# Performance work log

Measured on AMD Instinct MI355X. Metric: run time of the kernel, lower is better.

## Reference

```python
import jax, jax.numpy as jnp
import numpy as np

N, F_IN, H, OUT, E = 50000, 128, 128, 40, 800000


def setup_inputs() -> dict:
    key = jax.random.key(0)
    ks = jax.random.split(key, 20)
    s = 0.05
    return {
        "x": jax.random.normal(ks[0], (N, F_IN), jnp.float32),
        "edge_index": jax.random.randint(ks[1], (2, E), 0, N, jnp.int64),
        # GATConv (heads=1)
        "W_gat": jax.random.normal(ks[2], (F_IN, H), jnp.float32) * s,
        "att_src": jax.random.normal(ks[3], (H,), jnp.float32) * s,
        "att_dst": jax.random.normal(ks[4], (H,), jnp.float32) * s,
        "b_gat": jnp.zeros((H,), jnp.float32),
        # GCNConv
        "W_gcn": jax.random.normal(ks[5], (F_IN, H), jnp.float32) * s,
        "b_gcn": jnp.zeros((H,), jnp.float32),
        # SAGEConv (mean aggr): lin_l on neighbors (with bias), lin_r on root (no bias)
        "W_sage_l": jax.random.normal(ks[6], (F_IN, H), jnp.float32) * s,
        "b_sage_l": jnp.zeros((H,), jnp.float32),
        "W_sage_r": jax.random.normal(ks[7], (F_IN, H), jnp.float32) * s,
        # MLP head
        "W1": jax.random.normal(ks[8], (3 * H, 2 * H), jnp.float32) * s,
        "b1": jnp.zeros((2 * H,), jnp.float32),
        "W2": jax.random.normal(ks[9], (2 * H, H), jnp.float32) * s,
        "b2": jnp.zeros((H,), jnp.float32),
        "W3": jax.random.normal(ks[10], (H, OUT), jnp.float32) * s,
        "b3": jnp.zeros((OUT,), jnp.float32),
        # BatchNorm1d(3H)
        "gamma": jnp.ones((3 * H,), jnp.float32),
        "beta": jnp.zeros((3 * H,), jnp.float32),
    }


def _add_self_loops(edge_index, n):
    loop = jnp.arange(n, dtype=edge_index.dtype)
    src = jnp.concatenate([edge_index[0], loop])
    dst = jnp.concatenate([edge_index[1], loop])
    return src, dst


def _gat(x, src, dst, n, W, att_src, att_dst, bias):
    h = x @ W                                   # [N, H]
    a_s = h @ att_src                           # [N]
    a_d = h @ att_dst                           # [N]
    e = jax.nn.leaky_relu(a_s[src] + a_d[dst], 0.2)  # [E']
    m = jax.ops.segment_max(e, dst, num_segments=n)
    ex = jnp.exp(e - m[dst])
    denom = jax.ops.segment_sum(ex, dst, num_segments=n)
    alpha = ex / denom[dst]
    out = jax.ops.segment_sum(alpha[:, None] * h[src], dst, num_segments=n)
    return out + bias


def _gcn(x, src, dst, n, W, bias):
    h = x @ W
    deg = jax.ops.segment_sum(jnp.ones_like(dst, dtype=h.dtype), dst, num_segments=n)
    dinv = jnp.where(deg > 0, jax.lax.rsqrt(deg), 0.0)
    norm = dinv[src] * dinv[dst]                # [E']
    out = jax.ops.segment_sum(norm[:, None] * h[src], dst, num_segments=n)
    return out + bias


def _sage(x, src, dst, n, W_l, b_l, W_r):
    agg = jax.ops.segment_sum(x[src], dst, num_segments=n)
    cnt = jax.ops.segment_sum(jnp.ones_like(dst, dtype=x.dtype), dst, num_segments=n)
    mean = agg / jnp.maximum(cnt, 1.0)[:, None]
    return mean @ W_l + b_l + x @ W_r


def reference(x, edge_index, W_gat, att_src, att_dst, b_gat, W_gcn, b_gcn,
              W_sage_l, b_sage_l, W_sage_r, W1, b1, W2, b2, W3, b3, gamma, beta):
    n = x.shape[0]
    src, dst = edge_index[0], edge_index[1]          # SAGE: no self-loops
    src_sl, dst_sl = _add_self_loops(edge_index, n)  # GAT/GCN add self-loops

    x_gat = _gat(x, src_sl, dst_sl, n, W_gat, att_src, att_dst, b_gat)
    x_gcn = _gcn(x, src_sl, dst_sl, n, W_gcn, b_gcn)
    x_sage = _sage(x, src, dst, n, W_sage_l, b_sage_l, W_sage_r)

    h = jnp.concatenate([x_gat, x_gcn, x_sage], axis=1)  # [N, 3H]
    # BatchNorm1d (training-mode batch statistics; biased variance, eps=1e-5)
    mu = h.mean(axis=0)
    var = h.var(axis=0)
    h = (h - mu) * jax.lax.rsqrt(var + 1e-5) * gamma + beta
    # dropout is identity at inference
    h = jax.nn.relu(h) @ W1 + b1
    h = jax.nn.relu(h) @ W2 + b2
    h = jax.nn.relu(h) @ W3 + b3
    return h
```

## Files before the change

### kernel.cpp

```cpp
#include <hip/hip_runtime.h>
#include <cstdint>
#include <cstddef>

#define NN   50000
#define FIN  128
#define HD   128
#define EE   800000
#define C3   384
#define NOUT 40

#define SC_ELEMS 512
#define SC_BLKS  ((NN + SC_ELEMS - 1) / SC_ELEMS)
#define NBLK ((NN + 127) / 128)

#define SPLIT_BLKS ((NN + 3) / 4)

#define NBUCK ((NN + 511) / 512)
#define BCAP  16384
#define BK_BLKS ((EE + 8191) / 8192)
#define SCAP  12288

#define LDSW 132

typedef __attribute__((ext_vector_type(8))) short s8v;
typedef __attribute__((ext_vector_type(4))) float f4v;
typedef __attribute__((ext_vector_type(4))) ushort u4v;

typedef const __attribute__((address_space(1))) unsigned int* guintp;
typedef __attribute__((address_space(3))) unsigned int* luintp;

static __device__ __forceinline__ void async_copy16(const void* g, void* l) {
    __builtin_amdgcn_global_load_lds((guintp)g, (luintp)l, 16, 0, 0);
}

static __device__ __forceinline__ float b2f(ushort u) {
    return __uint_as_float((unsigned)u << 16);
}
static __device__ __forceinline__ ushort f2b(float v) {
    unsigned u = __float_as_uint(v);
    unsigned r = u + 0x7fffu + ((u >> 16) & 1u);
    return (ushort)(r >> 16);
}

__global__ __launch_bounds__(256) void k_split_x_att(
    const float* __restrict__ x,
    const float* __restrict__ w_as, const float* __restrict__ w_ad,
    ushort* __restrict__ xb,
    float* __restrict__ a_s, float* __restrict__ a_d)
{
    int node = blockIdx.x * 4 + (threadIdx.x >> 6);
    if (node >= NN) return;
    int lane = threadIdx.x & 63;
    size_t o = (size_t)node * 128 + lane * 2;
    float2 v  = *(const float2*)(x + o);
    { ushort2 u; u.x = f2b(v.x); u.y = f2b(v.y); *(ushort2*)(xb + o) = u; }
    float2 w1 = *(const float2*)(w_as + lane * 2);
    float2 w2 = *(const float2*)(w_ad + lane * 2);
    float s1 = v.x * w1.x + v.y * w1.y;
    float s2 = v.x * w2.x + v.y * w2.y;
    #pragma unroll
    for (int off = 32; off; off >>= 1) {
        s1 += __shfl_down(s1, off);
        s2 += __shfl_down(s2, off);
    }
    if (lane == 0) { a_s[node] = s1; a_d[node] = s2; }
}

__global__ void k_splitw_all(
    const float* __restrict__ Wg, const float* __restrict__ Wc,
    const float* __restrict__ Wl, const float* __restrict__ Wr,
    const float* __restrict__ W1, const float* __restrict__ W2,
    const float* __restrict__ W3,
    const float* __restrict__ asv, const float* __restrict__ adv,
    float* __restrict__ w_as, float* __restrict__ w_ad,
    ushort* __restrict__ btg, ushort* __restrict__ btc,
    ushort* __restrict__ btsg,
    ushort* __restrict__ bt1, ushort* __restrict__ bt2,
    ushort* __restrict__ bt3)
{
    int ry = blockIdx.x;
    int t = threadIdx.x;
    if (ry == 816) {
        if (t < 128) {
            float s1 = 0.f, s2 = 0.f;
            for (int j = 0; j < 128; ++j) {
                float w = Wg[t * 128 + j];
                s1 += w * asv[j];
                s2 += w * adv[j];
            }
            w_as[t] = s1; w_ad[t] = s2;
        }
        return;
    }
    const float* W = nullptr; ushort* dh; int K, Nw, n;
    bool sage = false;
    if (ry < 128)      { n = ry;       K = 128; Nw = 128; W = Wg; dh = btg; }
    else if (ry < 256) { n = ry - 128; K = 128; Nw = 128; W = Wc; dh = btc; }
    else if (ry < 384) { n = ry - 256; K = 256; Nw = 128; sage = true; dh = btsg; }
    else if (ry < 640) { n = ry - 384; K = 384; Nw = 256; W = W1; dh = bt1; }
    else if (ry < 768) { n = ry - 640; K = 256; Nw = 128; W = W2; dh = bt2; }
    else               { n = ry - 768; K = 128; Nw = 40;  W = W3; dh = bt3; }
    for (int k = t; k < K; k += 256) {
        float v;
        if (sage) v = (k < 128) ? Wl[(size_t)k * 128 + n] : Wr[(size_t)(k - 128) * 128 + n];
        else      v = (n < Nw) ? W[(size_t)k * Nw + n] : 0.f;
        dh[(size_t)n * K + k] = f2b(v);
    }
}

template<int NT, int NCH, int AX>
__global__ __launch_bounds__(256, 5) void k_gemm2(
    const ushort* __restrict__ A, int K,
    const ushort* __restrict__ Bt,
    int M, int mode,
    const float* __restrict__ bias,
    float* __restrict__ Cf, int ldc,
    ushort* __restrict__ Ch, int ldch,
    int colmax)
{
    constexpr int COLS = NT * 16;
    constexpr int HOPU = 8 * COLS;
    constexpr int KTOT = NCH * 128;

    __shared__ __align__(16) ushort S[16384];
    ushort* Bs = S;
    ushort* As = S + 8192;

    const int lane = threadIdx.x & 63;
    const int wave = threadIdx.x >> 6;
    const int quad = lane >> 4;
    const int ln15 = lane & 15;
    const int brow = AX ? blockIdx.y : blockIdx.x;
    const int bcol = AX ? blockIdx.x : blockIdx.y;
    const int row0 = brow * 128 + wave * 32;
    const int col0 = bcol * COLS;
    const int Rbase = brow * 128;

    auto stageB = [&](int c, int h) {
        for (int u0 = wave * 64; u0 < HOPU; u0 += 256) {
            int u  = u0 + lane;
            int kq  = u / COLS;
            int col = u - kq * COLS;
            int kk  = c * 128 + h * 64 + kq * 8;
            const ushort* gp = Bt + (size_t)(col0 + col) * KTOT + kk;
            async_copy16(gp, (char*)Bs + (size_t)u0 * 16);
        }
    };
    auto stageA = [&](int c, int h) {
        #pragma unroll
        for (int i = 0; i < 4; ++i) {
            int u0 = (wave * 4 + i) * 64;
            int u  = u0 + lane;
            int row = u >> 3;
            int s   = u & 7;
            int sg  = s ^ (row & 7);
            int rr = Rbase + row; if (rr > M - 1) rr = M - 1;
            int kk = c * 128 + h * 64 + sg * 8;
            const ushort* gp = A + (size_t)rr * K + kk;
            async_copy16(gp, (char*)As + (size_t)u0 * 16);
        }
    };
    auto afrag = [&](int jj, int mt) -> s8v {
        int r = wave * 32 + mt * 16 + ln15;
        int sg = jj * 4 + quad;
        int unit = r * 8 + (sg ^ (r & 7));
        return *(const s8v*)(As + (size_t)unit * 8);
    };

    f4v acc[2][NT] = {};

    auto compute = [&](int jj) {
        s8v a0 = afrag(jj, 0);
        s8v a1 = afrag(jj, 1);
        #pragma unroll
        for (int t = 0; t < NT; ++t) {
            int ub = (jj * 4 + quad) * COLS + t * 16 + ln15;
            s8v b = *(const s8v*)(Bs + (size_t)ub * 8);
            acc[0][t] = __builtin_amdgcn_mfma_f32_16x16x32_bf16(a0, b, acc[0][t], 0, 0, 0);
            acc[1][t] = __builtin_amdgcn_mfma_f32_16x16x32_bf16(a1, b, acc[1][t], 0, 0, 0);
        }
    };

    stageB(0, 0); stageA(0, 0);
    __syncthreads();

    #pragma unroll
    for (int ph = 0; ph < NCH; ++ph) {
        #pragma unroll
        for (int h = 0; h < 2; ++h) {
            compute(0); compute(1);
            if (!(ph == NCH - 1 && h == 1)) {
                __syncthreads();
                int nc = ph, nh = h + 1;
                if (nh == 2) { nh = 0; ++nc; }
                stageB(nc, nh); stageA(nc, nh);
                __syncthreads();
            }
        }
    }

    if (NT == 8 && mode == 0) {
        __syncthreads();
        ushort* Lp = S + wave * 2176;
        #pragma unroll
        for (int mt = 0; mt < 2; ++mt) {
            #pragma unroll
            for (int t = 0; t < NT; ++t) {
                int cc = col0 + t * 16 + ln15;
                #pragma unroll
                for (int r = 0; r < 4; ++r) {
                    float v = acc[mt][t][r] + bias[cc];
                    v = v > 0.f ? v : 0.f;
                    Lp[(quad * 4 + r) * LDSW + t * 16 + ln15] = f2b(v);
                }
            }
            int cb = (lane & 31) * 4;
            #pragma unroll
            for (int it = 0; it < 8; ++it) {
                int row2 = it * 2 + (lane >> 5);
                int rr = row0 + mt * 16 + row2;
                uint2 v = *(uint2*)(Lp + row2 * LDSW + cb);
                if (rr < M)
                    *(uint2*)(Ch + (size_t)rr * ldch + col0 + cb) = v;
            }
        }
    } else {
        #pragma unroll
        for (int t = 0; t < NT; ++t) {
            int cc = col0 + t * 16 + ln15;
            #pragma unroll
            for (int mt = 0; mt < 2; ++mt) {
                #pragma unroll
                for (int r = 0; r < 4; ++r) {
                    int rr = row0 + mt * 16 + quad * 4 + r;
                    if (rr < M && cc < colmax)
                        Cf[(size_t)rr * ldc + cc] = acc[mt][t][r] + bias[cc];
                }
            }
        }
    }
}

__global__ __launch_bounds__(256, 3) void k_gemm_prod(
    const ushort* __restrict__ tgb, const ushort* __restrict__ tcb,
    const ushort* __restrict__ tsb, const ushort* __restrict__ xb,
    const ushort* __restrict__ btg, const ushort* __restrict__ btc,
    const ushort* __restrict__ btsg,
    const float* __restrict__ bg, const float* __restrict__ bc,
    const float* __restrict__ bsl,
    float* __restrict__ pS, float* __restrict__ pQ,
    ushort* __restrict__ hch)
{
    constexpr int COLS = 128;
    constexpr int HOPU = 8 * COLS;
    __shared__ __align__(16) ushort S[16384];
    ushort* Bs = S;
    ushort* As = S + 8192;
    float* red = (float*)(S + 14336);

    const int z = blockIdx.z;
    const ushort* A1 = (z == 0) ? tgb : (z == 1) ? tcb : tsb;
    const ushort* Bt = (z == 0) ? btg : (z == 1) ? btc : btsg;
    const float*  bias = (z == 0) ? bg : (z == 1) ? bc : bsl;
    const int nch = (z == 2) ? 2 : 1;
    const int ktot = nch * 128;

    const int lane = threadIdx.x & 63;
    const int wave = threadIdx.x >> 6;
    const int quad = lane >> 4;
    const int ln15 = lane & 15;
    const int row0 = blockIdx.x * 128 + wave * 32;
    const int Rbase = blockIdx.x * 128;

    auto stageB = [&](int c, int h) {
        for (int u0 = wave * 64; u0 < HOPU; u0 += 256) {
            int u  = u0 + lane;
            int kq  = u / COLS;
            int col = u - kq * COLS;
            int kk  = c * 128 + h * 64 + kq * 8;
            const ushort* gp = Bt + (size_t)col * ktot + kk;
            async_copy16(gp, (char*)Bs + (size_t)u0 * 16);
        }
    };
    auto stageA = [&](int c, int h) {
        #pragma unroll
        for (int i = 0; i < 4; ++i) {
            int u0 = (wave * 4 + i) * 64;
            int u  = u0 + lane;
            int row = u >> 3;
            int s   = u & 7;
            int sg  = s ^ (row & 7);
            int rr = Rbase + row; if (rr > NN - 1) rr = NN - 1;
            int kk = c * 128 + h * 64 + sg * 8;
            const ushort* gp = (kk < 128) ? (A1 + (size_t)rr * 128 + kk)
                                          : (xb + (size_t)rr * 128 + (kk - 128));
            async_copy16(gp, (char*)As + (size_t)u0 * 16);
        }
    };
    auto afrag = [&](int jj, int mt) -> s8v {
        int r = wave * 32 + mt * 16 + ln15;
        int sg = jj * 4 + quad;
        int unit = r * 8 + (sg ^ (r & 7));
        return *(const s8v*)(As + (size_t)unit * 8);
    };

    f4v acc[2][8] = {};

    auto compute = [&](int jj) {
        s8v a0 = afrag(jj, 0);
        s8v a1 = afrag(jj, 1);
        #pragma unroll
        for (int t = 0; t < 8; ++t) {
            int ub = (jj * 4 + quad) * COLS + t * 16 + ln15;
            s8v b = *(const s8v*)(Bs + (size_t)ub * 8);
            acc[0][t] = __builtin_amdgcn_mfma_f32_16x16x32_bf16(a0, b, acc[0][t], 0, 0, 0);
            acc[1][t] = __builtin_amdgcn_mfma_f32_16x16x32_bf16(a1, b, acc[1][t], 0, 0, 0);
        }
    };

    stageB(0, 0); stageA(0, 0);
    __syncthreads();

    for (int ph = 0; ph < nch; ++ph) {
        for (int h = 0; h < 2; ++h) {
            compute(0); compute(1);
            if (!(ph == nch - 1 && h == 1)) {
                __syncthreads();
                int nc = ph, nh = h + 1;
                if (nh == 2) { nh = 0; ++nc; }
                stageB(nc, nh); stageA(nc, nh);
                __syncthreads();
            }
        }
    }

    __syncthreads();
    if (threadIdx.x < 256) red[threadIdx.x] = 0.f;
    ushort* Lp = S + wave * 2176;
    float sp[8] = {}, qp[8] = {};
    #pragma unroll
    for (int mt = 0; mt < 2; ++mt) {
        #pragma unroll
        for (int t = 0; t < 8; ++t) {
            #pragma unroll
            for (int r = 0; r < 4; ++r) {
                int rr = row0 + mt * 16 + quad * 4 + r;
                float v = acc[mt][t][r] + bias[t * 16 + ln15];
                Lp[(quad * 4 + r) * LDSW + t * 16 + ln15] = f2b(v);
                if (rr < NN) { sp[t] += v; qp[t] += v * v; }
            }
        }
        int cb = (lane & 31) * 4;
        #pragma unroll
        for (int it = 0; it < 8; ++it) {
            int row2 = it * 2 + (lane >> 5);
            int rr = row0 + mt * 16 + row2;
            uint2 v = *(uint2*)(Lp + row2 * LDSW + cb);
            if (rr < NN)
                *(uint2*)(hch + (size_t)rr * C3 + z * 128 + cb) = v;
        }
    }
    __syncthreads();
    #pragma unroll
    for (int t = 0; t < 8; ++t) {
        float s = sp[t], q = qp[t];
        s += __shfl_xor(s, 16); s += __shfl_xor(s, 32);
        q += __shfl_xor(q, 16); q += __shfl_xor(q, 32);
        if (quad == 0) {
            atomicAdd(&red[t * 16 + ln15], s);
            atomicAdd(&red[128 + t * 16 + ln15], q);
        }
    }
    __syncthreads();
    if (threadIdx.x < 128) {
        size_t o = (size_t)blockIdx.x * C3 + z * 128 + threadIdx.x;
        pS[o] = red[threadIdx.x];
        pQ[o] = red[128 + threadIdx.x];
    }
}

__global__ __launch_bounds__(256) void k_scan_part(
    const int* __restrict__ degA, int* __restrict__ bsum)
{
    int t = threadIdx.x;
    int b0 = blockIdx.x * SC_ELEMS;
    int i0 = b0 + t * 2;
    int v0 = (i0 < NN)     ? degA[i0] + 1     : 0;
    int v1 = (i0 + 1 < NN) ? degA[i0 + 1] + 1 : 0;
    int s = v0 + v1;
    #pragma unroll
    for (int off = 32; off; off >>= 1) s += __shfl_down(s, off);
    __shared__ int ws[4];
    if ((t & 63) == 0) ws[t >> 6] = s;
    __syncthreads();
    if (t == 0) bsum[blockIdx.x] = ws[0] + ws[1] + ws[2] + ws[3];
}

__global__ __launch_bounds__(128) void k_scan_tops(
    const int* __restrict__ bsum, int* __restrict__ boffs)
{
    __shared__ int sh[128];
    int t = threadIdx.x;
    int v = (t < SC_BLKS) ? bsum[t] : 0;
    sh[t] = v;
    __syncthreads();
    for (int off = 1; off < 128; off <<= 1) {
        int u = (t >= off) ? sh[t - off] : 0;
        __syncthreads();
        sh[t] += u;
        __syncthreads();
    }
    if (t < SC_BLKS) boffs[t] = sh[t] - v;
    if (t == SC_BLKS - 1) boffs[SC_BLKS] = sh[t];
}

__global__ __launch_bounds__(256) void k_scan_apply(
    const int* __restrict__ degA, const int* __restrict__ boffs,
    int* __restrict__ offs, float* __restrict__ dinv)
{
    __shared__ int sh[256];
    int t = threadIdx.x;
    int b0 = blockIdx.x * SC_ELEMS;
    int i0 = b0 + t * 2;
    int v0 = (i0 < NN)     ? degA[i0] + 1     : 0;
    int v1 = (i0 + 1 < NN) ? degA[i0 + 1] + 1 : 0;
    int pair = v0 + v1;
    sh[t] = pair;
    __syncthreads();
    for (int off = 1; off < 256; off <<= 1) {
        int u = (t >= off) ? sh[t - off] : 0;
        __syncthreads();
        sh[t] += u;
        __syncthreads();
    }
    int excl = sh[t] - pair + boffs[blockIdx.x];
    if (i0 < NN) {
        offs[i0] = excl;
        dinv[i0] = rsqrtf((float)v0);
    }
    if (i0 + 1 < NN) {
        offs[i0 + 1] = excl + v0;
        dinv[i0 + 1] = rsqrtf((float)v1);
    }
    if (blockIdx.x == SC_BLKS - 1 && t == 255) offs[NN] = excl + pair;
}

__global__ __launch_bounds__(1024) void k_bucket(
    const int* __restrict__ e_src, const int* __restrict__ e_dst,
    int* __restrict__ bcnt, uint* __restrict__ ebuf)
{
    __shared__ uint sval[8192];
    __shared__ int scnt[NBUCK], sbase[NBUCK];
    int t = threadIdx.x;
    if (t < NBUCK) scnt[t] = 0;
    __syncthreads();
    int e0 = blockIdx.x * 8192;
    #pragma unroll
    for (int i = 0; i < 8; ++i) {
        int g = e0 + i * 1024 + t;
        uint val = 0xffffffffu;
        if (g < EE) {
            int d = e_dst[g];
            int s = e_src[g];
            int b = d >> 9;
            val = ((uint)b << 25) | ((uint)(d & 511) << 16) | (uint)s;
            atomicAdd(&scnt[b], 1);
        }
        sval[i * 1024 + t] = val;
    }
    __syncthreads();
    if (t < NBUCK) {
        sbase[t] = atomicAdd(&bcnt[t], scnt[t]);
        scnt[t] = 0;
    }
    __syncthreads();
    #pragma unroll
    for (int i = 0; i < 8; ++i) {
        uint val = sval[i * 1024 + t];
        if (val != 0xffffffffu) {
            int b = val >> 25;
            int lo = atomicAdd(&scnt[b], 1);
            ebuf[(size_t)b * BCAP + sbase[b] + lo] = val;
        }
    }
}

__global__ __launch_bounds__(1024) void k_deg(
    const int* __restrict__ bcnt, const uint* __restrict__ ebuf,
    int* __restrict__ degA)
{
    __shared__ int hist[512];
    int b = blockIdx.x, t = threadIdx.x;
    int d0 = b * 512;
    int ndst = NN - d0; if (ndst > 512) ndst = 512;
    if (t < 512) hist[t] = 0;
    __syncthreads();
    int nb = bcnt[b];
    const uint* eb = ebuf + (size_t)b * BCAP;
    for (int i = t; i < nb; i += 1024)
        atomicAdd(&hist[(eb[i] >> 16) & 511], 1);
    __syncthreads();
    if (t < ndst) degA[d0 + t] = hist[t];
}

__global__ __launch_bounds__(1024) void k_csr_build(
    const int* __restrict__ bcnt, const uint* __restrict__ ebuf,
    const int* __restrict__ offs, ushort* __restrict__ esrc)
{
    __shared__ ushort sout[SCAP];
    __shared__ int cur[512];
    int b = blockIdx.x, t = threadIdx.x;
    int d0 = b * 512;
    int ndst = NN - d0; if (ndst > 512) ndst = 512;
    int obase = offs[d0];
    if (t < ndst) cur[t] = offs[d0 + t] - obase;
    __syncthreads();
    int nb = bcnt[b];
    const uint* eb = ebuf + (size_t)b * BCAP;
    for (int i = t; i < nb; i += 1024) {
        uint val = eb[i];
        int slot = atomicAdd(&cur[(val >> 16) & 511], 1);
        sout[slot] = (ushort)(val & 0xffffu);
    }
    if (t < ndst) {
        int slot = atomicAdd(&cur[t], 1);
        sout[slot] = (ushort)(d0 + t);
    }
    __syncthreads();
    int total = offs[d0 + ndst] - obase;
    for (int i = t; i < total; i += 1024)
        esrc[obase + i] = sout[i];
}

__global__ __launch_bounds__(256) void k_gather(
    const ushort* __restrict__ esrc, const int* __restrict__ offs,
    const float* __restrict__ a_s, const float* __restrict__ a_d,
    const float* __restrict__ dinv,
    const ushort* __restrict__ xb,
    ushort* __restrict__ tgb, ushort* __restrict__ tcb,
    ushort* __restrict__ tsb)
{
    int d = blockIdx.x * 4 + (threadIdx.x >> 6);
    if (d >= NN) return;
    int lane = threadIdx.x & 63;
    int sub = lane & 31;
    int grp = lane >> 5;
    int beg = offs[d], end = offs[d + 1];
    float ad = a_d[d], dd = dinv[d];

    int idx0 = beg + lane;
    bool v0 = idx0 < end;
    int s0 = d; float e0 = 0.f, wc0 = 0.f;
    if (v0) {
        s0 = esrc[idx0];
        float e = a_s[s0] + ad;
        e0 = (e > 0.f) ? e : 0.2f * e;
        wc0 = dinv[s0] * dd;
    }
    float m = v0 ? e0 : -3.0e38f;
    for (int base = beg + 64; base < end; base += 64) {
        int idx = base + lane;
        if (idx < end) {
            int s = esrc[idx];
            float e = a_s[s] + ad;
            e = (e > 0.f) ? e : 0.2f * e;
            m = fmaxf(m, e);
        }
    }
    #pragma unroll
    for (int off = 1; off < 64; off <<= 1) m = fmaxf(m, __shfl_xor(m, off));
    float ex0 = v0 ? expf(e0 - m) : 0.f;
    float den = ex0;
    for (int base = beg + 64; base < end; base += 64) {
        int idx = base + lane;
        if (idx < end) {
            int s = esrc[idx];
            float e = a_s[s] + ad;
            e = (e > 0.f) ? e : 0.2f * e;
            den += expf(e - m);
        }
    }
    #pragma unroll
    for (int off = 1; off < 64; off <<= 1) den += __shfl_xor(den, off);
    float rden = 1.f / den;

    float tg[4] = {0.f, 0.f, 0.f, 0.f};
    float tc[4] = {0.f, 0.f, 0.f, 0.f};
    float ts[4] = {0.f, 0.f, 0.f, 0.f};

    const ushort* xbs = xb + sub * 4;

    auto fmacc = [&](u4v x4, uint pw, float vs) {
        float wg = __uint_as_float(pw << 16);
        float wc = __uint_as_float(pw & 0xffff0000u);
        #pragma unroll
        for (int k = 0; k < 4; ++k) {
            float xv = b2f(x4[k]);
            tg[k] += wg * xv;
            tc[k] += wc * xv;
            ts[k] += vs * xv;
        }
    };

    auto accum_batch = [&](int sreg, uint pwreg, int cb) {
        int j0 = grp;
        int sa = __shfl(sreg, j0);
        uint pa = (uint)__shfl((int)pwreg, j0);
        float va = (j0 < cb) ? 1.f : 0.f;
        u4v xa = *(const u4v*)(xbs + (size_t)sa * 128);

        int j1 = 2 + grp;
        int sb = __shfl(sreg, j1);
        uint pb = (uint)__shfl((int)pwreg, j1);
        float vb = (j1 < cb) ? 1.f : 0.f;
        u4v xc = *(const u4v*)(xbs + (size_t)sb * 128);

        for (int j = 4; j < cb; j += 2) {
            int jn = j + grp;
            int sn = __shfl(sreg, jn);
            uint pn = (uint)__shfl((int)pwreg, jn);
            float vn = (jn < cb) ? 1.f : 0.f;
            u4v xn = *(const u4v*)(xbs + (size_t)sn * 128);
            fmacc(xa, pa, va);
            xa = xc; pa = pb; va = vb;
            xc = xn; pb = pn; vb = vn;
        }
        fmacc(xa, pa, va);
        fmacc(xc, pb, vb);
    };

    {
        float wg = ex0 * rden;
        uint pw0 = (uint)f2b(wg) | ((uint)f2b(wc0) << 16);
        int cnt = end - beg; if (cnt > 64) cnt = 64;
        accum_batch(s0, pw0, cnt);
    }
    for (int base = beg + 64; base < end; base += 64) {
        int idx = base + lane;
        int s = d; uint pw = 0;
        if (idx < end) {
            s = esrc[idx];
            float e = a_s[s] + ad;
            e = (e > 0.f) ? e : 0.2f * e;
            float wg = expf(e - m) * rden;
            float wc = dinv[s] * dd;
            pw = (uint)f2b(wg) | ((uint)f2b(wc) << 16);
        }
        int cb = end - base; if (cb > 64) cb = 64;
        accum_batch(s, pw, cb);
    }

    #pragma unroll
    for (int k = 0; k < 4; ++k) {
        tg[k] += __shfl_xor(tg[k], 32);
        tc[k] += __shfl_xor(tc[k], 32);
        ts[k] += __shfl_xor(ts[k], 32);
    }
    if (lane < 32) {
        u4v xd = *(const u4v*)(xb + (size_t)d * 128 + lane * 4);
        int cs = (end - beg) - 1;
        float rc = 1.f / (float)(cs > 1 ? cs : 1);
        u4v og, oc, os;
        #pragma unroll
        for (int k = 0; k < 4; ++k) {
            og[k] = f2b(tg[k]);
            oc[k] = f2b(tc[k]);
            os[k] = f2b((ts[k] - b2f(xd[k])) * rc);
        }
        size_t row = (size_t)d * 128 + lane * 4;
        *(u4v*)(tgb + row) = og;
        *(u4v*)(tcb + row) = oc;
        *(u4v*)(tsb + row) = os;
    }
}

__global__ void k_bn_final(const float* __restrict__ pS, const float* __restrict__ pQ,
                           const float* __restrict__ gamma, const float* __restrict__ beta,
                           float* __restrict__ scale, float* __restrict__ shift)
{
    int j = blockIdx.x * 64 + threadIdx.x;
    if (j >= C3) return;
    float s = 0.f, q = 0.f;
    for (int r = 0; r < NBLK; ++r) {
        s += pS[(size_t)r * C3 + j];
        q += pQ[(size_t)r * C3 + j];
    }
    const float rn = 1.f / (float)NN;
    float mu  = s * rn;
    float var = q * rn - mu * mu;
    float sc  = gamma[j] * rsqrtf(var + 1e-5f);
    scale[j] = sc;
    shift[j] = beta[j] - mu * sc;
}

__global__ __launch_bounds__(256) void k_bnrelu(
    ushort* __restrict__ hch,
    const float* __restrict__ scale, const float* __restrict__ shift)
{
    int p = blockIdx.x * blockDim.x + threadIdx.x;
    if (p >= NN * 48) return;
    int cidx = (p % 48) * 8;
    size_t o = (size_t)p * 8;
    uint4 w = *(uint4*)(hch + o);
    uint wr[4] = {w.x, w.y, w.z, w.w};
    uint out[4];
    #pragma unroll
    for (int i = 0; i < 4; ++i) {
        ushort u0 = (ushort)(wr[i] & 0xffffu), u1 = (ushort)(wr[i] >> 16);
        int cc = cidx + i * 2;
        float v0 = b2f(u0) * scale[cc]     + shift[cc];
        float v1 = b2f(u1) * scale[cc + 1] + shift[cc + 1];
        v0 = v0 > 0.f ? v0 : 0.f;
        v1 = v1 > 0.f ? v1 : 0.f;
        out[i] = (uint)f2b(v0) | ((uint)f2b(v1) << 16);
    }
    uint4 r; r.x = out[0]; r.y = out[1]; r.z = out[2]; r.w = out[3];
    *(uint4*)(hch + o) = r;
}

extern "C" void kernel_launch(void* const* d_in, const int* in_sizes, int n_in,
                              void* d_out, int out_size, void* d_ws, size_t ws_size,
                              hipStream_t stream) {
    const float* x        = (const float*)d_in[0];
    const int*   ei       = (const int*)d_in[1];
    const float* W_gat    = (const float*)d_in[2];
    const float* att_src  = (const float*)d_in[3];
    const float* att_dst  = (const float*)d_in[4];
    const float* b_gat    = (const float*)d_in[5];
    const float* W_gcn    = (const float*)d_in[6];
    const float* b_gcn    = (const float*)d_in[7];
    const float* W_sage_l = (const float*)d_in[8];
    const float* b_sage_l = (const float*)d_in[9];
    const float* W_sage_r = (const float*)d_in[10];
    const float* W1       = (const float*)d_in[11];
    const float* b1       = (const float*)d_in[12];
    const float* W2       = (const float*)d_in[13];
    const float* b2       = (const float*)d_in[14];
    const float* W3       = (const float*)d_in[15];
    const float* b3       = (const float*)d_in[16];
    const float* gamma    = (const float*)d_in[17];
    const float* beta     = (const float*)d_in[18];

    const int* e_src = ei;
    const int* e_dst = ei + EE;

    char* base = (char*)d_ws;
    size_t o = 0;
    ushort* hch  = (ushort*)(base + o); o += (size_t)NN * C3 * 2;
    ushort* tgb  = (ushort*)(base + o); o += (size_t)NN * 128 * 2;
    ushort* tcb  = (ushort*)(base + o); o += (size_t)NN * 128 * 2;
    ushort* tsb  = (ushort*)(base + o); o += (size_t)NN * 128 * 2;
    ushort* xb   = (ushort*)(base + o); o += (size_t)NN * 128 * 2;
    ushort* esrc = (ushort*)(base + o); o += ((size_t)(EE + NN) * 2 + 15) & ~15ull;
    int*    offs = (int*)(base + o);    o += (size_t)(NN + 16) * 4;
    float*  as_  = (float*)(base + o);  o += (size_t)NN * 4;
    float*  ad_  = (float*)(base + o);  o += (size_t)NN * 4;
    float*  dinv = (float*)(base + o);  o += (size_t)NN * 4;
    int*    bsum = (int*)(base + o);    o += 256 * 4;
    int*    boffs= (int*)(base + o);    o += 256 * 4;
    int*    degA = (int*)(base + o);    o += (size_t)NN * 4;
    int*    bcnt = (int*)(base + o);    o += 128 * 4;
    float*  pS   = (float*)(base + o);  o += (size_t)NBLK * C3 * 4;
    float*  pQ   = (float*)(base + o);  o += (size_t)NBLK * C3 * 4;
    float*  scale= (float*)(base + o);  o += C3 * 4;
    float*  shift= (float*)(base + o);  o += C3 * 4;
    float*  w_as = (float*)(base + o);  o += 128 * 4;
    float*  w_ad = (float*)(base + o);  o += 128 * 4;
    ushort* btg  = (ushort*)(base + o); o += 128 * 128 * 2;
    ushort* btc  = (ushort*)(base + o); o += 128 * 128 * 2;
    ushort* btsg = (ushort*)(base + o); o += 128 * 256 * 2;
    ushort* bt1  = (ushort*)(base + o); o += 256 * 384 * 2;
    ushort* bt2  = (ushort*)(base + o); o += 128 * 256 * 2;
    ushort* bt3  = (ushort*)(base + o); o += 48 * 128 * 2;
    ushort* a1 = tgb;
    ushort* a2 = tsb;
    uint*   ebuf = (uint*)hch;

    hipMemsetAsync(bcnt, 0, 128 * 4, stream);

    k_splitw_all<<<817, 256, 0, stream>>>(W_gat, W_gcn, W_sage_l, W_sage_r, W1, W2, W3,
        att_src, att_dst, w_as, w_ad, btg, btc, btsg, bt1, bt2, bt3);
    k_split_x_att<<<SPLIT_BLKS, 256, 0, stream>>>(x, w_as, w_ad, xb, as_, ad_);

    k_bucket<<<BK_BLKS, 1024, 0, stream>>>(e_src, e_dst, bcnt, ebuf);
    k_deg<<<NBUCK, 1024, 0, stream>>>(bcnt, ebuf, degA);
    k_scan_part<<<SC_BLKS, 256, 0, stream>>>(degA, bsum);
    k_scan_tops<<<1, 128, 0, stream>>>(bsum, boffs);
    k_scan_apply<<<SC_BLKS, 256, 0, stream>>>(degA, boffs, offs, dinv);
    k_csr_build<<<NBUCK, 1024, 0, stream>>>(bcnt, ebuf, offs, esrc);

    k_gather<<<(NN + 3) / 4, 256, 0, stream>>>(
        esrc, offs, as_, ad_, dinv, xb, tgb, tcb, tsb);

    k_gemm_prod<<<dim3(NBLK, 1, 3), 256, 0, stream>>>(
        tgb, tcb, tsb, xb, btg, btc, btsg,
        b_gat, b_gcn, b_sage_l, pS, pQ, hch);

    k_bn_final<<<6, 64, 0, stream>>>(pS, pQ, gamma, beta, scale, shift);
    k_bnrelu<<<(NN * 48 + 255) / 256, 256, 0, stream>>>(hch, scale, shift);

    k_gemm2<8, 3, 1><<<dim3(2, NBLK), 256, 0, stream>>>(
        hch, 384, bt1, NN, 0, b1, nullptr, 0, a1, 256, 256);
    k_gemm2<8, 2, 0><<<dim3(NBLK, 1), 256, 0, stream>>>(
        a1, 256, bt2, NN, 0, b2, nullptr, 0, a2, 128, 128);
    k_gemm2<3, 1, 0><<<dim3(NBLK, 1), 256, 0, stream>>>(
        a2, 128, bt3, NN, 2, b3, (float*)d_out, NOUT, nullptr, 0, NOUT);
}
```

Baseline: 334.9 us.

## Cache per-edge attention records in LDS and pad gather with zero row

The gather kernel now computes each edge's leaky-relu score, source index and packed GCN weight once and stores them in a per-wave LDS buffer of up to 252 records. The softmax denominator and the weighting pass then read that buffer instead of re-gathering esrc, a_s and dinv on every pass. A zero row is appended to the bf16 copy of x, so padded slots read zeros and the inner loop needs no validity masks. The aggregation loop is rewritten as a double-buffered two-stage pipeline over those records. The cost is 8 KB of LDS per block and a separate fallback path for nodes with more than 252 edges.

```diff
diff --git a/kernel.cpp b/kernel.cpp
--- a/kernel.cpp
+++ b/kernel.cpp
@@ -13,12 +13,15 @@
 #define SC_BLKS  ((NN + SC_ELEMS - 1) / SC_ELEMS)
 #define NBLK ((NN + 127) / 128)
 
-#define SPLIT_BLKS ((NN + 3) / 4)
+#define SPLIT_BLKS ((NN + 4) / 4)
 
 #define NBUCK ((NN + 511) / 512)
 #define BCAP  16384
 #define BK_BLKS ((EE + 8191) / 8192)
 #define SCAP  12288
+
+#define REC_CAP 252
+#define ZROW NN
 
 #define LDSW 132
 
@@ -49,9 +52,14 @@
     float* __restrict__ a_s, float* __restrict__ a_d)
 {
     int node = blockIdx.x * 4 + (threadIdx.x >> 6);
-    if (node >= NN) return;
+    if (node > NN) return;
     int lane = threadIdx.x & 63;
     size_t o = (size_t)node * 128 + lane * 2;
+    if (node == NN) {
+        ushort2 z; z.x = 0; z.y = 0;
+        *(ushort2*)(xb + o) = z;
+        return;
+    }
     float2 v  = *(const float2*)(x + o);
     { ushort2 u; u.x = f2b(v.x); u.y = f2b(v.y); *(ushort2*)(xb + o) = u; }
     float2 w1 = *(const float2*)(w_as + lane * 2);
@@ -540,57 +548,77 @@
     ushort* __restrict__ tgb, ushort* __restrict__ tcb,
     ushort* __restrict__ tsb)
 {
-    int d = blockIdx.x * 4 + (threadIdx.x >> 6);
+    __shared__ uint2 recs[4][256];
+    int wv = threadIdx.x >> 6;
+    int d = blockIdx.x * 4 + wv;
     if (d >= NN) return;
     int lane = threadIdx.x & 63;
     int sub = lane & 31;
     int grp = lane >> 5;
+    uint2* rec = recs[wv];
     int beg = offs[d], end = offs[d + 1];
+    int cnt = end - beg;
     float ad = a_d[d], dd = dinv[d];
-
-    int idx0 = beg + lane;
-    bool v0 = idx0 < end;
-    int s0 = d; float e0 = 0.f, wc0 = 0.f;
-    if (v0) {
-        s0 = esrc[idx0];
-        float e = a_s[s0] + ad;
-        e0 = (e > 0.f) ? e : 0.2f * e;
-        wc0 = dinv[s0] * dd;
-    }
-    float m = v0 ? e0 : -3.0e38f;
-    for (int base = beg + 64; base < end; base += 64) {
-        int idx = base + lane;
+    int stored = cnt < REC_CAP ? cnt : REC_CAP;
+
+    float mloc = -3.0e38f;
+    for (int b = 0; b < cnt; b += 64) {
+        int j = b + lane;
+        int idx = beg + j;
         if (idx < end) {
             int s = esrc[idx];
             float e = a_s[s] + ad;
             e = (e > 0.f) ? e : 0.2f * e;
-            m = fmaxf(m, e);
-        }
-    }
+            mloc = fmaxf(mloc, e);
+            if (j < REC_CAP) {
+                uint2 r;
+                r.x = __float_as_uint(e);
+                r.y = (uint)s | ((uint)f2b(dinv[s] * dd) << 16);
+                rec[j] = r;
+            }
+        }
+    }
+    float m = mloc;
     #pragma unroll
     for (int off = 1; off < 64; off <<= 1) m = fmaxf(m, __shfl_xor(m, off));
-    float ex0 = v0 ? expf(e0 - m) : 0.f;
-    float den = ex0;
-    for (int base = beg + 64; base < end; base += 64) {
-        int idx = base + lane;
-        if (idx < end) {
-            int s = esrc[idx];
-            float e = a_s[s] + ad;
-            e = (e > 0.f) ? e : 0.2f * e;
-            den += expf(e - m);
-        }
-    }
+
+    float denl = 0.f;
+    for (int j = lane; j < stored; j += 64) {
+        float ex = expf(__uint_as_float(rec[j].x) - m);
+        denl += ex;
+        rec[j].x = __float_as_uint(ex);
+    }
+    for (int idx = beg + REC_CAP + lane; idx < end; idx += 64) {
+        int s = esrc[idx];
+        float e = a_s[s] + ad;
+        e = (e > 0.f) ? e : 0.2f * e;
+        denl += expf(e - m);
+    }
+    float den = denl;
     #pragma unroll
     for (int off = 1; off < 64; off <<= 1) den += __shfl_xor(den, off);
     float rden = 1.f / den;
 
-    float tg[4] = {0.f, 0.f, 0.f, 0.f};
-    float tc[4] = {0.f, 0.f, 0.f, 0.f};
-    float ts[4] = {0.f, 0.f, 0.f, 0.f};
-
+    for (int j = lane; j < stored; j += 64) {
+        uint2 r = rec[j];
+        float wg = __uint_as_float(r.x) * rden;
+        uint2 q;
+        q.x = (uint)f2b(wg) | (r.y & 0xffff0000u);
+        q.y = r.y & 0xffffu;
+        rec[j] = q;
+    }
+    int Pcnt = (stored + 3) & ~3;
+    if (lane < Pcnt + 4 - stored) {
+        uint2 q; q.x = 0u; q.y = (uint)ZROW;
+        rec[stored + lane] = q;
+    }
+
+    float tg[4] = {}, tc[4] = {}, ts[4] = {};
     const ushort* xbs = xb + sub * 4;
-
-    auto fmacc = [&](u4v x4, uint pw, float vs) {
+    auto ldx = [&](uint srow) -> u4v {
+        return *(const u4v*)(xbs + (size_t)srow * 128);
+    };
+    auto fmacc = [&](u4v x4, uint pw) {
         float wg = __uint_as_float(pw << 16);
         float wc = __uint_as_float(pw & 0xffff0000u);
         #pragma unroll
@@ -598,56 +626,46 @@
             float xv = b2f(x4[k]);
             tg[k] += wg * xv;
             tc[k] += wc * xv;
-            ts[k] += vs * xv;
-        }
-    };
-
-    auto accum_batch = [&](int sreg, uint pwreg, int cb) {
-        int j0 = grp;
-        int sa = __shfl(sreg, j0);
-        uint pa = (uint)__shfl((int)pwreg, j0);
-        float va = (j0 < cb) ? 1.f : 0.f;
-        u4v xa = *(const u4v*)(xbs + (size_t)sa * 128);
-
-        int j1 = 2 + grp;
-        int sb = __shfl(sreg, j1);
-        uint pb = (uint)__shfl((int)pwreg, j1);
-        float vb = (j1 < cb) ? 1.f : 0.f;
-        u4v xc = *(const u4v*)(xbs + (size_t)sb * 128);
-
-        for (int j = 4; j < cb; j += 2) {
-            int jn = j + grp;
-            int sn = __shfl(sreg, jn);
-            uint pn = (uint)__shfl((int)pwreg, jn);
-            float vn = (jn < cb) ? 1.f : 0.f;
-            u4v xn = *(const u4v*)(xbs + (size_t)sn * 128);
-            fmacc(xa, pa, va);
-            xa = xc; pa = pb; va = vb;
-            xc = xn; pb = pn; vb = vn;
-        }
-        fmacc(xa, pa, va);
-        fmacc(xc, pb, vb);
-    };
-
-    {
-        float wg = ex0 * rden;
-        uint pw0 = (uint)f2b(wg) | ((uint)f2b(wc0) << 16);
-        int cnt = end - beg; if (cnt > 64) cnt = 64;
-        accum_batch(s0, pw0, cnt);
-    }
-    for (int base = beg + 64; base < end; base += 64) {
+            ts[k] += xv;
+        }
+    };
+
+    int mB = Pcnt >> 2;
+    uint2 rA0 = rec[grp],     rA1 = rec[2 + grp];
+    u4v   xA0 = ldx(rA0.y),   xA1 = ldx(rA1.y);
+    uint2 rB0, rB1; u4v xB0, xB1;
+    int i = 0;
+    for (;;) {
+        rB0 = rec[4 * i + 4 + grp]; xB0 = ldx(rB0.y);
+        rB1 = rec[4 * i + 6 + grp]; xB1 = ldx(rB1.y);
+        fmacc(xA0, rA0.x); fmacc(xA1, rA1.x);
+        if (++i >= mB) break;
+        rA0 = rec[4 * i + 4 + grp]; xA0 = ldx(rA0.y);
+        rA1 = rec[4 * i + 6 + grp]; xA1 = ldx(rA1.y);
+        fmacc(xB0, rB0.x); fmacc(xB1, rB1.x);
+        if (++i >= mB) break;
+    }
+
+    for (int base = beg + REC_CAP; base < end; base += 64) {
         int idx = base + lane;
-        int s = d; uint pw = 0;
+        int s = ZROW; uint pw = 0;
         if (idx < end) {
-            s = esrc[idx];
-            float e = a_s[s] + ad;
+            int ss = esrc[idx];
+            float e = a_s[ss] + ad;
             e = (e > 0.f) ? e : 0.2f * e;
-            float wg = expf(e - m) * rden;
-            float wc = dinv[s] * dd;
-            pw = (uint)f2b(wg) | ((uint)f2b(wc) << 16);
+            pw = (uint)f2b(expf(e - m) * rden) | ((uint)f2b(dinv[ss] * dd) << 16);
+            s = ss;
         }
         int cb = end - base; if (cb > 64) cb = 64;
-        accum_batch(s, pw, cb);
+        for (int j = 0; j < cb; j += 2) {
+            int jj = j + grp;
+            int sa = __shfl(s, jj);
+            uint pa = (uint)__shfl((int)pw, jj);
+            bool vv = jj < cb;
+            sa = vv ? sa : ZROW;
+            pa = vv ? pa : 0u;
+            fmacc(ldx((uint)sa), pa);
+        }
     }
 
     #pragma unroll
@@ -658,7 +676,7 @@
     }
     if (lane < 32) {
         u4v xd = *(const u4v*)(xb + (size_t)d * 128 + lane * 4);
-        int cs = (end - beg) - 1;
+        int cs = cnt - 1;
         float rc = 1.f / (float)(cs > 1 ? cs : 1);
         u4v og, oc, os;
         #pragma unroll
@@ -750,7 +768,7 @@
     ushort* tgb  = (ushort*)(base + o); o += (size_t)NN * 128 * 2;
     ushort* tcb  = (ushort*)(base + o); o += (size_t)NN * 128 * 2;
     ushort* tsb  = (ushort*)(base + o); o += (size_t)NN * 128 * 2;
-    ushort* xb   = (ushort*)(base + o); o += (size_t)NN * 128 * 2;
+    ushort* xb   = (ushort*)(base + o); o += (size_t)(NN + 1) * 128 * 2;
     ushort* esrc = (ushort*)(base + o); o += ((size_t)(EE + NN) * 2 + 15) & ~15ull;
     int*    offs = (int*)(base + o);    o += (size_t)(NN + 16) * 4;
     float*  as_  = (float*)(base + o);  o += (size_t)NN * 4;
```

Measured after the change: 335.9 us. No clear change (+0.3%).
